# Kernel tuning notes

Hardware: AMD Instinct MI355X
Metric: run time of the kernel (lower is better)

## Reference

```python
import jax, jax.numpy as jnp
import numpy as np

B, N, F_IN = 4, 256, 64
ALPHA = 0.2  # leaky_relu negative slope
NEG = -9e15


def gat_layer(nf, edges, wp, bp, a, wa, ba, num_heads):
    """Faithful GATLayer (deterministic=True so dropout is identity).
    nf: [b, n] or [b, n, c_in]; edges: [B, N, N].
    """
    b, n = nf.shape[0], nf.shape[1]
    # to_adj: Dense(num_nodes) over last axis, sigmoid, symmetrize, hard threshold
    adj = jax.nn.sigmoid(edges @ wa + ba)              # [B, N, N]
    adj = (adj + jnp.swapaxes(adj, -1, -2)) * 0.5
    adj = (adj > 0.5).astype(jnp.float32)
    h = (nf @ wp + bp).reshape(b, n, num_heads, -1)    # [b, n, H, d]
    # NOTE: replicates source bug -- split index is a.shape[0]//2 == num_heads//2
    split = a.shape[0] // 2
    lp = (h * a[None, None, :, :split]).sum(-1)        # [b, n, H]
    lc = (h * a[None, None, :, split:]).sum(-1)        # [b, n, H]
    logits = jax.nn.leaky_relu(lp[:, :, None, :] + lc[:, None, :, :], ALPHA)
    logits = jnp.where(adj[..., None] == 1.0, logits, NEG)
    p = jax.nn.softmax(logits, axis=2)                 # softmax over child axis
    out = jnp.einsum('bijh,bjhc->bihc', p, h)
    return out.reshape(b, n, -1)                       # concat heads


def setup_inputs() -> dict:
    key = jax.random.key(0)
    ks = jax.random.split(key, 16)
    g = lambda i, shape, s=0.1: jax.random.normal(ks[i], shape, jnp.float32) * s
    return {
        'nodes': jax.random.normal(ks[0], (B, N, F_IN), jnp.float32),
        'edges': jax.random.normal(ks[1], (B, N, N), jnp.float32),
        # node layer 0: c_out=8, heads=4, c_in=F_IN
        'wp_n0': g(2, (F_IN, 8)), 'bp_n0': jnp.zeros(8, jnp.float32), 'a_n0': g(3, (4, 4), 0.5),
        'wadj_n0': g(4, (N, N)), 'badj_n0': jnp.zeros(N, jnp.float32),
        # edge layer 0: c_out=N, heads=1
        'wp_e0': g(5, (N, N)), 'bp_e0': jnp.zeros(N, jnp.float32), 'a_e0': g(6, (1, 2 * N), 0.05),
        'wadj_e0': g(7, (N, N)), 'badj_e0': jnp.zeros(N, jnp.float32),
        # node layer 1: c_in=8
        'wp_n1': g(8, (8, 8), 0.5), 'bp_n1': jnp.zeros(8, jnp.float32), 'a_n1': g(9, (4, 4), 0.5),
        'wadj_n1': g(10, (N, N)), 'badj_n1': jnp.zeros(N, jnp.float32),
        # edge layer 1
        'wp_e1': g(11, (N, N)), 'bp_e1': jnp.zeros(N, jnp.float32), 'a_e1': g(12, (1, 2 * N), 0.05),
        'wadj_e1': g(13, (N, N)), 'badj_e1': jnp.zeros(N, jnp.float32),
    }


def reference(nodes, edges,
              wp_n0, bp_n0, a_n0, wadj_n0, badj_n0,
              wp_e0, bp_e0, a_e0, wadj_e0, badj_e0,
              wp_n1, bp_n1, a_n1, wadj_n1, badj_n1,
              wp_e1, bp_e1, a_e1, wadj_e1, badj_e1):
    node_p = [(wp_n0, bp_n0, a_n0, wadj_n0, badj_n0),
              (wp_n1, bp_n1, a_n1, wadj_n1, badj_n1)]
    edge_p = [(wp_e0, bp_e0, a_e0, wadj_e0, badj_e0),
              (wp_e1, bp_e1, a_e1, wadj_e1, badj_e1)]
    for i in range(2):
        wp, bp, a, wa, ba = node_p[i]
        nodes = gat_layer(nodes, edges, wp, bp, a, wa, ba, num_heads=4)
        wpe, bpe, ae, wae, bae = edge_p[i]
        e_cur = edges
        edges = jax.vmap(
            lambda x: gat_layer(x, e_cur, wpe, bpe, ae, wae, bae, num_heads=1)[..., 0],
            in_axes=1, out_axes=1)(e_cur)
        edges = (edges + jnp.swapaxes(edges, 1, 2)) * 0.5
    # Source overwrites nodes with tanh(edges) (nodes.mean is dead code)
    out = jnp.tanh(edges)
    return out, out
```

## Files before the change

kernel.cpp:

```cpp
#include <hip/hip_runtime.h>
#include <math.h>

#define NB 4
#define NN 256
#define MAT (NN*NN)
#define BMAT (NB*MAT)
#define ALPHA 0.2f

typedef __attribute__((ext_vector_type(8))) __bf16 bf16x8;
typedef __attribute__((ext_vector_type(4))) float f32x4;

union U8 { bf16x8 v; unsigned short u[8]; };

#define MFMA(acc, A, B) acc = __builtin_amdgcn_mfma_f32_16x16x32_bf16(A, B, acc, 0, 0, 0)

__device__ __forceinline__ unsigned short f2bf(float x) {
    unsigned u = __float_as_uint(x);
    u = (u + 0x7FFFu + ((u >> 16) & 1u)) >> 16;
    return (unsigned short)u;
}
__device__ __forceinline__ float bf2f(unsigned short h) {
    return __uint_as_float(((unsigned)h) << 16);
}
__device__ __forceinline__ void split3(float x, unsigned short& a,
                                       unsigned short& b, unsigned short& c) {
    a = f2bf(x); float r = x - bf2f(a);
    b = f2bf(r); r -= bf2f(b);
    c = f2bf(r);
}

__device__ __forceinline__ float wave_sum(float v) {
#pragma unroll
    for (int o = 32; o > 0; o >>= 1) v += __shfl_down(v, o, 64);
    return v;
}
__device__ __forceinline__ float block_sum256(float v, volatile float* red) {
    int lane = threadIdx.x & 63, w = threadIdx.x >> 6;
    v = wave_sum(v);
    __syncthreads();
    if (lane == 0) red[w] = v;
    __syncthreads();
    return red[0] + red[1] + red[2] + red[3];
}

template<int L0>
__global__ __launch_bounds__(64) void k_gh(
    const float* __restrict__ Ef,
    const unsigned short* __restrict__ Epl,
    const float* __restrict__ Wa, const float* __restrict__ ba,
    const float* __restrict__ Wp, const float* __restrict__ bp,
    float* __restrict__ G, float* __restrict__ GT, float* __restrict__ H)
{
    int bid = blockIdx.x;
    int m = bid >> 10, b = (bid >> 8) & 3, t = bid & 255;
    int tm = t >> 4, tn = t & 15;
    const float* W = m ? Wp : Wa;
    const float* bias = m ? bp : ba;
    float* C = (m ? H : G) + b * MAT;
    int l = threadIdx.x, l15 = l & 15, lk = (l >> 4) * 8, lk4 = l >> 4;

    f32x4 acc = 0.0f;
    int arow = b * MAT + (tm * 16 + l15) * NN;
    int col = tn * 16 + l15;

    const int TP[6] = {0, 0, 1, 0, 1, 2}, TQ[6] = {0, 1, 0, 2, 1, 0};
#pragma unroll
    for (int k0 = 0; k0 < NN; k0 += 32) {
        int kb = k0 + lk;
        U8 aE[3], wv[3];
        if (L0) {
            f32x4 e0 = *(const f32x4*)&Ef[arow + kb];
            f32x4 e1 = *(const f32x4*)&Ef[arow + kb + 4];
#pragma unroll
            for (int i = 0; i < 4; ++i) {
                split3(e0[i], aE[0].u[i], aE[1].u[i], aE[2].u[i]);
                split3(e1[i], aE[0].u[i + 4], aE[1].u[i + 4], aE[2].u[i + 4]);
            }
        } else {
#pragma unroll
            for (int pp = 0; pp < 3; ++pp)
                aE[pp].v = *(const bf16x8*)&Epl[pp * BMAT + arow + kb];
        }
#pragma unroll
        for (int kk = 0; kk < 8; ++kk) {
            float wf = W[(kb + kk) * NN + col];
            split3(wf, wv[0].u[kk], wv[1].u[kk], wv[2].u[kk]);
        }
#pragma unroll
        for (int t6 = 0; t6 < 6; ++t6)
            MFMA(acc, aE[TP[t6]].v, wv[TQ[t6]].v);
    }
    float bv = bias[col];
#pragma unroll
    for (int r = 0; r < 4; ++r) {
        int row = tm * 16 + lk4 * 4 + r;
        C[row * NN + col] = acc[r] + bv;
    }
    if (m == 0) {
        f32x4 tv;
#pragma unroll
        for (int r = 0; r < 4; ++r) tv[r] = acc[r] + bv;
        *(f32x4*)&GT[b * MAT + col * NN + tm * 16 + lk4 * 4] = tv;
    }
}

template<int FINAL>
__global__ __launch_bounds__(256) void k_fsP(
    const float* __restrict__ G, const float* __restrict__ GT,
    const float* __restrict__ H, const float* __restrict__ ae,
    unsigned short* __restrict__ Epl, float* __restrict__ out)
{
    __shared__ float Fs[2][16 * 17];
    __shared__ float lst[2][2][16], hst[2][2][16], cst[2][2][16];
    __shared__ f32x4 pD[4][64], pN[4][64];
    __shared__ float red[4];
    int b = blockIdx.y;
    int ti = 0, rem = blockIdx.x;
    while (rem >= 16 - ti) { rem -= 16 - ti; ++ti; }
    int tj = ti + rem;
    int t = threadIdx.x, w = t >> 6, lane = t & 63, l15 = lane & 15, q = lane >> 4;
    int side = w >> 1, half = w & 1;
    int R = side ? tj : ti, C = side ? ti : tj;

    float S = block_sum256(ae[t] + ae[t + 256], red);

    float hrow[4][8];
    int hbase = b * MAT + (R * 16 + l15) * NN + half * 128;
    float lmax = -3.4e38f, hsum = 0.f;
#pragma unroll
    for (int it = 0; it < 4; ++it) {
        f32x4 h0 = *(const f32x4*)&H[hbase + it * 32 + q * 8];
        f32x4 h1 = *(const f32x4*)&H[hbase + it * 32 + q * 8 + 4];
#pragma unroll
        for (int i = 0; i < 4; ++i) { hrow[it][i] = h0[i]; hrow[it][i + 4] = h1[i]; }
#pragma unroll
        for (int i = 0; i < 8; ++i) {
            float x = S * hrow[it][i];
            float L = (x > 0.f) ? x : ALPHA * x;
            lmax = fmaxf(lmax, L);
            hsum += hrow[it][i];
        }
    }
    lmax = fmaxf(lmax, __shfl_xor(lmax, 16, 64));
    lmax = fmaxf(lmax, __shfl_xor(lmax, 32, 64));
    hsum += __shfl_xor(hsum, 16, 64);
    hsum += __shfl_xor(hsum, 32, 64);
    if (q == 0) { lst[side][half][l15] = lmax; hst[side][half][l15] = hsum; }

    float cntp = 0.f;
    bf16x8 adjf[4];
    int gbase = b * MAT + (C * 16 + l15) * NN + half * 128;
#pragma unroll
    for (int it = 0; it < 4; ++it) {
        f32x4 g0 = *(const f32x4*)&G[gbase + it * 32 + q * 8];
        f32x4 g1 = *(const f32x4*)&G[gbase + it * 32 + q * 8 + 4];
        f32x4 t0 = *(const f32x4*)&GT[gbase + it * 32 + q * 8];
        f32x4 t1 = *(const f32x4*)&GT[gbase + it * 32 + q * 8 + 4];
        U8 a_;
#pragma unroll
        for (int i = 0; i < 4; ++i) {
            bool b0 = (g0[i] + t0[i] > 0.f);
            bool b1 = (g1[i] + t1[i] > 0.f);
            cntp += (b0 ? 1.f : 0.f) + (b1 ? 1.f : 0.f);
            a_.u[i] = b0 ? 0x3F80 : 0;
            a_.u[i + 4] = b1 ? 0x3F80 : 0;
        }
        adjf[it] = a_.v;
    }
    cntp += __shfl_xor(cntp, 16, 64);
    cntp += __shfl_xor(cntp, 32, 64);
    if (q == 0) cst[side][half][l15] = cntp;
    __syncthreads();

    float lmaxC = fmaxf(lst[side][0][l15], lst[side][1][l15]);

    f32x4 aD = 0.f, aN = 0.f;
#pragma unroll
    for (int it = 0; it < 4; ++it) {
        U8 e0, e1, e2, q0, q1, q2;
#pragma unroll
        for (int i = 0; i < 8; ++i) {
            float x = S * hrow[it][i];
            float L = (x > 0.f) ? x : ALPHA * x;
            float e = __expf(L - lmaxC);
            float eh = e * hrow[it][i];
            split3(e,  e0.u[i], e1.u[i], e2.u[i]);
            split3(eh, q0.u[i], q1.u[i], q2.u[i]);
        }
        MFMA(aD, e0.v, adjf[it]); MFMA(aD, e1.v, adjf[it]); MFMA(aD, e2.v, adjf[it]);
        MFMA(aN, q0.v, adjf[it]); MFMA(aN, q1.v, adjf[it]); MFMA(aN, q2.v, adjf[it]);
    }
    pD[w][lane] = aD;
    pN[w][lane] = aN;
    __syncthreads();

    float F[4] = {0.f, 0.f, 0.f, 0.f};
    if (half == 0) {
        float cntC = cst[side][0][l15] + cst[side][1][l15];
#pragma unroll
        for (int r = 0; r < 4; ++r) {
            int m = q * 4 + r;
            float dv = pD[2 * side][lane][r] + pD[2 * side + 1][lane][r];
            float nv = pN[2 * side][lane][r] + pN[2 * side + 1][lane][r];
            float rsv = (hst[side][0][m] + hst[side][1][m]) * (1.f / 256.f);
            F[r] = (cntC > 0.5f) ? nv / dv : rsv;
            Fs[side][m * 17 + l15] = F[r];
        }
    }
    __syncthreads();
    if (half == 0) {
#pragma unroll
        for (int r = 0; r < 4; ++r) {
            int m = q * 4 + r;
            float e = 0.5f * (F[r] + Fs[1 ^ side][l15 * 17 + m]);
            int idx = b * MAT + (R * 16 + m) * NN + C * 16 + l15;
            if (FINAL) {
                float tv = tanhf(e);
                out[idx] = tv; out[BMAT + idx] = tv;
            } else {
                unsigned short s0, s1, s2;
                split3(e, s0, s1, s2);
                Epl[idx] = s0; Epl[BMAT + idx] = s1; Epl[2 * BMAT + idx] = s2;
            }
        }
    }
}

extern "C" void kernel_launch(void* const* d_in, const int* in_sizes, int n_in,
                              void* d_out, int out_size, void* d_ws, size_t ws_size,
                              hipStream_t stream) {
    const float* edges = (const float*)d_in[1];
    const float* wp[2] = {(const float*)d_in[7],  (const float*)d_in[17]};
    const float* bp[2] = {(const float*)d_in[8],  (const float*)d_in[18]};
    const float* ae[2] = {(const float*)d_in[9],  (const float*)d_in[19]};
    const float* wa[2] = {(const float*)d_in[10], (const float*)d_in[20]};
    const float* ba[2] = {(const float*)d_in[11], (const float*)d_in[21]};
    float* out = (float*)d_out;

    unsigned short* EplB = (unsigned short*)d_ws;
    float* G  = (float*)(EplB + 3 * BMAT);
    float* GT = G + BMAT;
    float* H  = GT + BMAT;

    k_gh<1><<<2048, 64, 0, stream>>>(edges, nullptr, wa[0], ba[0], wp[0], bp[0],
                                     G, GT, H);
    k_fsP<0><<<dim3(136, NB), 256, 0, stream>>>(G, GT, H, ae[0], EplB, nullptr);
    k_gh<0><<<2048, 64, 0, stream>>>(nullptr, EplB, wa[1], ba[1], wp[1], bp[1],
                                     G, GT, H);
    k_fsP<1><<<dim3(136, NB), 256, 0, stream>>>(G, GT, H, ae[1], nullptr, out);
}
```

Measured before the change: 58.60 us.

## Split K across waves in GEMM and fused softmax kernels for more parallelism

```diff
diff --git a/kernel.cpp b/kernel.cpp
--- a/kernel.cpp
+++ b/kernel.cpp
@@ -29,35 +29,29 @@
     c = f2bf(r);
 }
 
-__device__ __forceinline__ float wave_sum(float v) {
-#pragma unroll
-    for (int o = 32; o > 0; o >>= 1) v += __shfl_down(v, o, 64);
+__device__ __forceinline__ float wave_allsum(float v) {
+#pragma unroll
+    for (int o = 1; o < 64; o <<= 1) v += __shfl_xor(v, o, 64);
     return v;
 }
-__device__ __forceinline__ float block_sum256(float v, volatile float* red) {
-    int lane = threadIdx.x & 63, w = threadIdx.x >> 6;
-    v = wave_sum(v);
-    __syncthreads();
-    if (lane == 0) red[w] = v;
-    __syncthreads();
-    return red[0] + red[1] + red[2] + red[3];
-}
 
 template<int L0>
-__global__ __launch_bounds__(64) void k_gh(
+__global__ __launch_bounds__(128) void k_gh(
     const float* __restrict__ Ef,
     const unsigned short* __restrict__ Epl,
     const float* __restrict__ Wa, const float* __restrict__ ba,
     const float* __restrict__ Wp, const float* __restrict__ bp,
     float* __restrict__ G, float* __restrict__ GT, float* __restrict__ H)
 {
+    __shared__ f32x4 part[64];
     int bid = blockIdx.x;
     int m = bid >> 10, b = (bid >> 8) & 3, t = bid & 255;
     int tm = t >> 4, tn = t & 15;
     const float* W = m ? Wp : Wa;
     const float* bias = m ? bp : ba;
     float* C = (m ? H : G) + b * MAT;
-    int l = threadIdx.x, l15 = l & 15, lk = (l >> 4) * 8, lk4 = l >> 4;
+    int tid = threadIdx.x, h = tid >> 6, lane = tid & 63;
+    int l15 = lane & 15, lk = (lane >> 4) * 8, lk4 = lane >> 4;
 
     f32x4 acc = 0.0f;
     int arow = b * MAT + (tm * 16 + l15) * NN;
@@ -65,8 +59,8 @@
 
     const int TP[6] = {0, 0, 1, 0, 1, 2}, TQ[6] = {0, 1, 0, 2, 1, 0};
 #pragma unroll
-    for (int k0 = 0; k0 < NN; k0 += 32) {
-        int kb = k0 + lk;
+    for (int ks = 0; ks < 4; ++ks) {
+        int kb = h * 128 + ks * 32 + lk;
         U8 aE[3], wv[3];
         if (L0) {
             f32x4 e0 = *(const f32x4*)&Ef[arow + kb];
@@ -90,45 +84,49 @@
         for (int t6 = 0; t6 < 6; ++t6)
             MFMA(acc, aE[TP[t6]].v, wv[TQ[t6]].v);
     }
-    float bv = bias[col];
-#pragma unroll
-    for (int r = 0; r < 4; ++r) {
-        int row = tm * 16 + lk4 * 4 + r;
-        C[row * NN + col] = acc[r] + bv;
-    }
-    if (m == 0) {
+    if (h == 1) part[lane] = acc;
+    __syncthreads();
+    if (h == 0) {
+        f32x4 hi = part[lane];
+        float bv = bias[col];
         f32x4 tv;
 #pragma unroll
-        for (int r = 0; r < 4; ++r) tv[r] = acc[r] + bv;
-        *(f32x4*)&GT[b * MAT + col * NN + tm * 16 + lk4 * 4] = tv;
+        for (int r = 0; r < 4; ++r) tv[r] = (acc[r] + hi[r]) + bv;
+#pragma unroll
+        for (int r = 0; r < 4; ++r)
+            C[(tm * 16 + lk4 * 4 + r) * NN + col] = tv[r];
+        if (m == 0)
+            *(f32x4*)&GT[b * MAT + col * NN + tm * 16 + lk4 * 4] = tv;
     }
 }
 
 template<int FINAL>
-__global__ __launch_bounds__(256) void k_fsP(
+__global__ __launch_bounds__(512) void k_fsP(
     const float* __restrict__ G, const float* __restrict__ GT,
     const float* __restrict__ H, const float* __restrict__ ae,
     unsigned short* __restrict__ Epl, float* __restrict__ out)
 {
     __shared__ float Fs[2][16 * 17];
-    __shared__ float lst[2][2][16], hst[2][2][16], cst[2][2][16];
-    __shared__ f32x4 pD[4][64], pN[4][64];
-    __shared__ float red[4];
+    __shared__ float lst[2][4][16], hst[2][4][16], cst[2][4][16];
+    __shared__ f32x4 pD[8][64], pN[8][64];
     int b = blockIdx.y;
     int ti = 0, rem = blockIdx.x;
     while (rem >= 16 - ti) { rem -= 16 - ti; ++ti; }
     int tj = ti + rem;
     int t = threadIdx.x, w = t >> 6, lane = t & 63, l15 = lane & 15, q = lane >> 4;
-    int side = w >> 1, half = w & 1;
+    int side = w >> 2, quar = w & 3;
     int R = side ? tj : ti, C = side ? ti : tj;
 
-    float S = block_sum256(ae[t] + ae[t + 256], red);
-
-    float hrow[4][8];
-    int hbase = b * MAT + (R * 16 + l15) * NN + half * 128;
+    float sv = 0.f;
+#pragma unroll
+    for (int k = 0; k < 8; ++k) sv += ae[lane + 64 * k];
+    float S = wave_allsum(sv);
+
+    float hrow[2][8];
+    int hbase = b * MAT + (R * 16 + l15) * NN + quar * 64;
     float lmax = -3.4e38f, hsum = 0.f;
 #pragma unroll
-    for (int it = 0; it < 4; ++it) {
+    for (int it = 0; it < 2; ++it) {
         f32x4 h0 = *(const f32x4*)&H[hbase + it * 32 + q * 8];
         f32x4 h1 = *(const f32x4*)&H[hbase + it * 32 + q * 8 + 4];
 #pragma unroll
@@ -145,13 +143,13 @@
     lmax = fmaxf(lmax, __shfl_xor(lmax, 32, 64));
     hsum += __shfl_xor(hsum, 16, 64);
     hsum += __shfl_xor(hsum, 32, 64);
-    if (q == 0) { lst[side][half][l15] = lmax; hst[side][half][l15] = hsum; }
+    if (q == 0) { lst[side][quar][l15] = lmax; hst[side][quar][l15] = hsum; }
 
     float cntp = 0.f;
-    bf16x8 adjf[4];
-    int gbase = b * MAT + (C * 16 + l15) * NN + half * 128;
-#pragma unroll
-    for (int it = 0; it < 4; ++it) {
+    bf16x8 adjf[2];
+    int gbase = b * MAT + (C * 16 + l15) * NN + quar * 64;
+#pragma unroll
+    for (int it = 0; it < 2; ++it) {
         f32x4 g0 = *(const f32x4*)&G[gbase + it * 32 + q * 8];
         f32x4 g1 = *(const f32x4*)&G[gbase + it * 32 + q * 8 + 4];
         f32x4 t0 = *(const f32x4*)&GT[gbase + it * 32 + q * 8];
@@ -169,14 +167,15 @@
     }
     cntp += __shfl_xor(cntp, 16, 64);
     cntp += __shfl_xor(cntp, 32, 64);
-    if (q == 0) cst[side][half][l15] = cntp;
-    __syncthreads();
-
-    float lmaxC = fmaxf(lst[side][0][l15], lst[side][1][l15]);
+    if (q == 0) cst[side][quar][l15] = cntp;
+    __syncthreads();
+
+    float lmaxC = fmaxf(fmaxf(lst[side][0][l15], lst[side][1][l15]),
+                        fmaxf(lst[side][2][l15], lst[side][3][l15]));
 
     f32x4 aD = 0.f, aN = 0.f;
 #pragma unroll
-    for (int it = 0; it < 4; ++it) {
+    for (int it = 0; it < 2; ++it) {
         U8 e0, e1, e2, q0, q1, q2;
 #pragma unroll
         for (int i = 0; i < 8; ++i) {
@@ -195,20 +194,24 @@
     __syncthreads();
 
     float F[4] = {0.f, 0.f, 0.f, 0.f};
-    if (half == 0) {
-        float cntC = cst[side][0][l15] + cst[side][1][l15];
+    if (quar == 0) {
+        float cntC = ((cst[side][0][l15] + cst[side][1][l15]) +
+                      cst[side][2][l15]) + cst[side][3][l15];
 #pragma unroll
         for (int r = 0; r < 4; ++r) {
             int m = q * 4 + r;
-            float dv = pD[2 * side][lane][r] + pD[2 * side + 1][lane][r];
-            float nv = pN[2 * side][lane][r] + pN[2 * side + 1][lane][r];
-            float rsv = (hst[side][0][m] + hst[side][1][m]) * (1.f / 256.f);
+            float dv = ((pD[4*side][lane][r] + pD[4*side+1][lane][r]) +
+                        pD[4*side+2][lane][r]) + pD[4*side+3][lane][r];
+            float nv = ((pN[4*side][lane][r] + pN[4*side+1][lane][r]) +
+                        pN[4*side+2][lane][r]) + pN[4*side+3][lane][r];
+            float rsv = (((hst[side][0][m] + hst[side][1][m]) +
+                          hst[side][2][m]) + hst[side][3][m]) * (1.f / 256.f);
             F[r] = (cntC > 0.5f) ? nv / dv : rsv;
             Fs[side][m * 17 + l15] = F[r];
         }
     }
     __syncthreads();
-    if (half == 0) {
+    if (quar == 0) {
 #pragma unroll
         for (int r = 0; r < 4; ++r) {
             int m = q * 4 + r;
@@ -242,10 +245,10 @@
     float* GT = G + BMAT;
     float* H  = GT + BMAT;
 
-    k_gh<1><<<2048, 64, 0, stream>>>(edges, nullptr, wa[0], ba[0], wp[0], bp[0],
-                                     G, GT, H);
-    k_fsP<0><<<dim3(136, NB), 256, 0, stream>>>(G, GT, H, ae[0], EplB, nullptr);
-    k_gh<0><<<2048, 64, 0, stream>>>(nullptr, EplB, wa[1], ba[1], wp[1], bp[1],
-                                     G, GT, H);
-    k_fsP<1><<<dim3(136, NB), 256, 0, stream>>>(G, GT, H, ae[1], nullptr, out);
-}
+    k_gh<1><<<2048, 128, 0, stream>>>(edges, nullptr, wa[0], ba[0], wp[0], bp[0],
+                                      G, GT, H);
+    k_fsP<0><<<dim3(136, NB), 512, 0, stream>>>(G, GT, H, ae[0], EplB, nullptr);
+    k_gh<0><<<2048, 128, 0, stream>>>(nullptr, EplB, wa[1], ba[1], wp[1], bp[1],
+                                      G, GT, H);
+    k_fsP<1><<<dim3(136, NB), 512, 0, stream>>>(G, GT, H, ae[1], nullptr, out);
+}
```

After: 58.55 us. About the same (-0.1%).
